# Kernel optimization log

Hardware: AMD Instinct MI355X
Metric: run time of the kernel (lower is better)

Reference implementation:

```python
import jax, jax.numpy as jnp
import numpy as np

B, S, D_IN = 2, 2048, 2048
H, KVH, HD = 32, 8, 64
GROUPS = H // KVH
EPS = 1e-6
SCALE = HD ** -0.5


def setup_inputs() -> dict:
    key = jax.random.key(0)
    ks = jax.random.split(key, 6)
    x = jax.random.normal(ks[0], (B, S, D_IN), jnp.float32)
    Wq = jax.random.normal(ks[1], (H * HD, D_IN), jnp.float32) * 0.02
    Wk = jax.random.normal(ks[2], (KVH * HD, D_IN), jnp.float32) * 0.02
    Wv = jax.random.normal(ks[3], (KVH * HD, D_IN), jnp.float32) * 0.02
    Wo = jax.random.normal(ks[4], (D_IN, H * HD), jnp.float32) * 0.02
    w_qnorm = jnp.ones((HD,), jnp.float32)
    w_knorm = jnp.ones((HD,), jnp.float32)
    # Llama-style RoPE tables: [S, HD] with frequencies duplicated across halves
    inv_freq = 1.0 / (10000.0 ** (np.arange(0, HD, 2, dtype=np.float32) / HD))
    ang = np.outer(np.arange(S, dtype=np.float32), inv_freq)  # [S, HD/2]
    emb = np.concatenate([ang, ang], axis=-1)  # [S, HD]
    cos = jnp.asarray(np.cos(emb), jnp.float32)
    sin = jnp.asarray(np.sin(emb), jnp.float32)
    mask = jnp.tril(jnp.ones((S, S), jnp.bool_))  # unused by module (causal hardcoded)
    return dict(x=x, mask=mask, cos=cos, sin=sin, Wq=Wq, Wk=Wk, Wv=Wv, Wo=Wo,
                w_qnorm=w_qnorm, w_knorm=w_knorm)


def _rms_norm(t, w):
    # per-head-dim RMSNorm, eps inside sqrt (torch nn.RMSNorm semantics)
    var = jnp.mean(jnp.square(t), axis=-1, keepdims=True)
    return t * jax.lax.rsqrt(var + EPS) * w


def _rotate_half(t):
    t1, t2 = jnp.split(t, 2, axis=-1)
    return jnp.concatenate([-t2, t1], axis=-1)


def _rope(t, cos, sin):
    # t: [B,H,S,HD]; cos/sin: [S,HD]
    return t * cos[None, None] + _rotate_half(t) * sin[None, None]


def reference(x, mask, cos, sin, Wq, Wk, Wv, Wo, w_qnorm, w_knorm):
    bs, seq, _ = x.shape
    q = (x @ Wq.T).reshape(bs, seq, H, HD).transpose(0, 2, 1, 3)    # [B,H,S,hd]
    k = (x @ Wk.T).reshape(bs, seq, KVH, HD).transpose(0, 2, 1, 3)  # [B,KVH,S,hd]
    v = (x @ Wv.T).reshape(bs, seq, KVH, HD).transpose(0, 2, 1, 3)
    # GQA: repeat_interleave KV over head dim
    k = jnp.repeat(k, GROUPS, axis=1)
    v = jnp.repeat(v, GROUPS, axis=1)
    # fused QK RMSNorm then RoPE
    q = _rope(_rms_norm(q, w_qnorm), cos, sin)
    k = _rope(_rms_norm(k, w_knorm), cos, sin)
    # causal attention
    scores = jnp.einsum('bhqd,bhkd->bhqk', q, k) * SCALE
    causal = jnp.arange(seq)[:, None] >= jnp.arange(seq)[None, :]
    scores = jnp.where(causal, scores, jnp.finfo(scores.dtype).min)
    attn = jax.nn.softmax(scores, axis=-1)
    out = jnp.einsum('bhqk,bhkd->bhqd', attn, v)
    out = out.transpose(0, 2, 1, 3).reshape(bs, seq, H * HD)
    return out @ Wo.T
```

## Files before the change

### kernel.cpp

```cpp
#include <hip/hip_runtime.h>

typedef __bf16 bf16_t;
typedef __bf16 bf16x8 __attribute__((ext_vector_type(8)));
typedef __bf16 bf16x4 __attribute__((ext_vector_type(4)));
typedef float f32x4 __attribute__((ext_vector_type(4)));
typedef unsigned int u32;

#define AS1 __attribute__((address_space(1)))
#define AS3 __attribute__((address_space(3)))

#define ASTR 72

#if __has_builtin(__builtin_amdgcn_exp2f)
#define EXP2(x) __builtin_amdgcn_exp2f(x)
#else
#define EXP2(x) exp2f(x)
#endif

__device__ __forceinline__ void g2l16(const bf16_t* g, bf16_t* l) {
  __builtin_amdgcn_global_load_lds((const AS1 u32*)g, (AS3 u32*)l, 16, 0, 0);
}

__device__ __forceinline__ u32 pkbf(float a, float b) {
  u32 ua = __builtin_bit_cast(u32, a) + 0x8000u;
  u32 ub = __builtin_bit_cast(u32, b) + 0x8000u;
  return (ua >> 16) | (ub & 0xFFFF0000u);
}

__global__ __launch_bounds__(256) void cvt5(
    const float* __restrict__ s0, const float* __restrict__ s1,
    const float* __restrict__ s2, const float* __restrict__ s3,
    const float* __restrict__ s4,
    bf16_t* __restrict__ d0, bf16_t* __restrict__ d1, bf16_t* __restrict__ d2,
    bf16_t* __restrict__ d3, bf16_t* __restrict__ d4)
{
  int blk = blockIdx.x;
  const float* s; bf16_t* d; int off;
  if      (blk <  8192) { s = s0; d = d0; off = blk;         }
  else if (blk < 12288) { s = s1; d = d1; off = blk -  8192; }
  else if (blk < 13312) { s = s2; d = d2; off = blk - 12288; }
  else if (blk < 14336) { s = s3; d = d3; off = blk - 13312; }
  else                  { s = s4; d = d4; off = blk - 14336; }
  size_t i = (size_t)off * 1024 + threadIdx.x * 4;
  float4 v = *(const float4*)&s[i];
  bf16x4 t;
  t[0] = (bf16_t)v.x; t[1] = (bf16_t)v.y; t[2] = (bf16_t)v.z; t[3] = (bf16_t)v.w;
  *(bf16x4*)&d[i] = t;
}

__device__ __forceinline__ void gemm_core(
    const bf16_t* __restrict__ A, const bf16_t* __restrict__ B, int K,
    bf16_t* As0, bf16_t* As1, bf16_t* Bs0, bf16_t* Bs1, f32x4 (&acc)[4][4])
{
  const int tid = threadIdx.x, lane = tid & 63, w = tid >> 6;
  const int col = lane & 15, quad = lane >> 4;
  const int wm = w >> 1, wn = w & 1;
  const int lr = lane >> 2;
  const int lc = (((lane & 3) ^ ((lane >> 3) & 3)) << 3);
  const int sw = ((quad ^ ((col >> 1) & 3)) << 3);
  const bf16_t* ga = A + (size_t)(w * 16 + lr) * K + lc;
  const bf16_t* gb = B + (size_t)(w * 16 + lr) * K + lc;
  const int lo0 = (w * 16) * 32, lo1 = (64 + w * 16) * 32;

  g2l16(ga,                  As0 + lo0);
  g2l16(ga + (size_t)64 * K, As0 + lo1);
  g2l16(gb,                  Bs0 + lo0);
  g2l16(gb + (size_t)64 * K, Bs0 + lo1);

  const int nkb = K >> 5;
  for (int kb = 0; kb < nkb; ++kb) {
    __syncthreads();
    bf16_t* Ac = (kb & 1) ? As1 : As0;
    bf16_t* Bc = (kb & 1) ? Bs1 : Bs0;
    if (kb + 1 < nkb) {
      bf16_t* An = (kb & 1) ? As0 : As1;
      bf16_t* Bn = (kb & 1) ? Bs0 : Bs1;
      const int k2 = (kb + 1) * 32;
      g2l16(ga + k2,                  An + lo0);
      g2l16(ga + k2 + (size_t)64 * K, An + lo1);
      g2l16(gb + k2,                  Bn + lo0);
      g2l16(gb + k2 + (size_t)64 * K, Bn + lo1);
    }

    bf16x8 af[4], bfr[4];
#pragma unroll
    for (int mt = 0; mt < 4; ++mt)
      af[mt] = *(const bf16x8*)&Ac[(wm * 64 + mt * 16 + col) * 32 + sw];
#pragma unroll
    for (int nt = 0; nt < 4; ++nt)
      bfr[nt] = *(const bf16x8*)&Bc[(wn * 64 + nt * 16 + col) * 32 + sw];
#pragma unroll
    for (int mt = 0; mt < 4; ++mt)
#pragma unroll
      for (int nt = 0; nt < 4; ++nt)
        acc[mt][nt] = __builtin_amdgcn_mfma_f32_16x16x32_bf16(af[mt], bfr[nt], acc[mt][nt], 0, 0, 0);
  }
}

__global__ __launch_bounds__(256, 4) void gemm_qkv(
    const bf16_t* __restrict__ xb, const bf16_t* __restrict__ Wqb,
    const bf16_t* __restrict__ Wkb, const bf16_t* __restrict__ Wvb,
    const float* __restrict__ cosT, const float* __restrict__ sinT,
    const float* __restrict__ wq, const float* __restrict__ wk,
    bf16_t* __restrict__ Qn, bf16_t* __restrict__ Kn, bf16_t* __restrict__ Vp)
{
  __shared__ bf16_t As[2][128 * 32], Bs[2][128 * 32];
  const int bn = blockIdx.x, bm = blockIdx.y;
  const bf16_t* B;
  if      (bn < 16) B = Wqb + (size_t)bn * 128 * 2048;
  else if (bn < 20) B = Wkb + (size_t)(bn - 16) * 128 * 2048;
  else              B = Wvb + (size_t)(bn - 20) * 128 * 2048;

  f32x4 acc[4][4] = {};
  gemm_core(xb + (size_t)bm * 128 * 2048, B, 2048, As[0], As[1], Bs[0], Bs[1], acc);

  const int lane = threadIdx.x & 63, w = threadIdx.x >> 6;
  const int col = lane & 15, quad = lane >> 4, wm = w >> 1, wn = w & 1;

  if (bn < 20) {
    const bool isQ = bn < 16;
    const float* wnv = isQ ? wq : wk;
    float w4[4];
#pragma unroll
    for (int nt = 0; nt < 4; ++nt) w4[nt] = wnv[nt * 16 + col];
    bf16_t* dst = isQ ? Qn + ((size_t)(bn * 2 + wn)) * 2048 * 64
                      : Kn + ((size_t)((bn - 16) * 2 + wn)) * 2048 * 64;
    const size_t bstride = isQ ? (size_t)32 * 2048 * 64 : (size_t)8 * 2048 * 64;
    const float qscale = 0.125f * 1.4426950408889634f;

#pragma unroll
    for (int mt = 0; mt < 4; ++mt)
#pragma unroll
      for (int r = 0; r < 4; ++r) {
        int row = bm * 128 + wm * 64 + mt * 16 + quad * 4 + r;
        int b = row >> 11, s = row & 2047;
        float v[4], ss = 0.f;
#pragma unroll
        for (int nt = 0; nt < 4; ++nt) { v[nt] = acc[mt][nt][r]; ss += v[nt] * v[nt]; }
        ss += __shfl_xor(ss, 1, 64);
        ss += __shfl_xor(ss, 2, 64);
        ss += __shfl_xor(ss, 4, 64);
        ss += __shfl_xor(ss, 8, 64);
        float rr = rsqrtf(ss * (1.0f / 64.0f) + 1e-6f);
        float t[4];
#pragma unroll
        for (int nt = 0; nt < 4; ++nt) t[nt] = v[nt] * rr * w4[nt];
        bf16_t* drow = dst + b * bstride + (size_t)s * 64;
#pragma unroll
        for (int nt = 0; nt < 4; ++nt) {
          int hd = nt * 16 + col;
          float rot = (nt < 2) ? -t[nt + 2] : t[nt - 2];
          float ov = t[nt] * cosT[s * 64 + hd] + rot * sinT[s * 64 + hd];
          if (isQ) ov *= qscale;
          drow[hd] = (bf16_t)ov;
        }
      }
  } else {
    const int cb = (bn - 20) * 128;
#pragma unroll
    for (int mt = 0; mt < 4; ++mt)
#pragma unroll
      for (int r = 0; r < 4; ++r) {
        int row = bm * 128 + wm * 64 + mt * 16 + quad * 4 + r;
        bf16_t* crow = Vp + (size_t)row * 512 + cb + wn * 64 + col;
#pragma unroll
        for (int nt = 0; nt < 4; ++nt)
          crow[nt * 16] = (bf16_t)acc[mt][nt][r];
      }
  }
}

__global__ __launch_bounds__(256, 4) void gemm_o(
    const bf16_t* __restrict__ Ao, const bf16_t* __restrict__ Wob,
    float* __restrict__ Cf)
{
  __shared__ bf16_t As[2][128 * 32], Bs[2][128 * 32];
  const int bn = blockIdx.x, bm = blockIdx.y;
  f32x4 acc[4][4] = {};
  gemm_core(Ao + (size_t)bm * 128 * 2048, Wob + (size_t)bn * 128 * 2048, 2048,
            As[0], As[1], Bs[0], Bs[1], acc);

  const int lane = threadIdx.x & 63, w = threadIdx.x >> 6;
  const int col = lane & 15, quad = lane >> 4, wm = w >> 1, wn = w & 1;
#pragma unroll
  for (int mt = 0; mt < 4; ++mt)
#pragma unroll
    for (int r = 0; r < 4; ++r) {
      int row = bm * 128 + wm * 64 + mt * 16 + quad * 4 + r;
      float* crow = Cf + (size_t)row * 2048 + bn * 128 + wn * 64 + col;
#pragma unroll
      for (int nt = 0; nt < 4; ++nt)
        crow[nt * 16] = acc[mt][nt][r];
    }
}

__global__ __launch_bounds__(256) void vtrans(
    const bf16_t* __restrict__ Vp, bf16_t* __restrict__ Vt)
{
  __shared__ bf16_t T[64 * 136];
  const int st = blockIdx.x, kvh = blockIdx.y, b = blockIdx.z;
  const int tid = threadIdx.x;
#pragma unroll
  for (int p = 0; p < 4; ++p) {
    int r = p * 32 + (tid >> 3);
    int c = (tid & 7) * 8;
    bf16x8 v = *(const bf16x8*)&Vp[((size_t)(b * 2048 + st * 128 + r)) * 512 + kvh * 64 + c];
#pragma unroll
    for (int i = 0; i < 8; ++i) T[(c + i) * 136 + r] = v[i];
  }
  __syncthreads();
#pragma unroll
  for (int p = 0; p < 4; ++p) {
    int hd = p * 16 + (tid >> 4);
    int sc = (tid & 15) * 8;
    bf16x8 v = *(const bf16x8*)&T[hd * 136 + sc];
    *(bf16x8*)&Vt[((size_t)((b * 8 + kvh) * 64) + hd) * 2048 + st * 128 + sc] = v;
  }
}

__global__ __launch_bounds__(256, 3) void attn(
    const bf16_t* __restrict__ Qn, const bf16_t* __restrict__ Kn,
    const bf16_t* __restrict__ Vt, bf16_t* __restrict__ Ao)
{
  __shared__ bf16_t KsL[2][64 * 32], KsH[2][64 * 32];
  __shared__ bf16_t VsL[2][64 * 32], VsH[2][64 * 32];
  __shared__ bf16_t Ps[128 * ASTR];

  const int tid = threadIdx.x, lane = tid & 63, w = tid >> 6;
  const int col = lane & 15, quad = lane >> 4;
  const int lr = lane >> 2;
  const int lcs = (((lane & 3) ^ ((lane >> 3) & 3)) << 3);
  const int sw  = ((quad ^ ((col >> 1) & 3)) << 3);
  const int h = blockIdx.x, b = blockIdx.y;
  const int qt = 15 - blockIdx.z;
  const int kvh = h >> 2;

  const bf16_t* Kb = Kn + ((size_t)(b * 8 + kvh)) * 2048 * 64;
  const bf16_t* Vb = Vt + ((size_t)(b * 8 + kvh)) * 64 * 2048;
  const bf16_t* Qb = Qn + (((size_t)(b * 32 + h)) * 2048 + qt * 128) * 64;
  const int lw = w * 512;

  bf16x8 Qf[2][2];
#pragma unroll
  for (int mt = 0; mt < 2; ++mt)
#pragma unroll
    for (int kk = 0; kk < 2; ++kk)
      Qf[mt][kk] = *(const bf16x8*)&Qb[(w * 32 + mt * 16 + col) * 64 + kk * 32 + quad * 8];

  bf16x8 ones;
#pragma unroll
  for (int i = 0; i < 8; ++i) ones[i] = (bf16_t)1.0f;

  f32x4 o[2][4] = {};
  f32x4 lacc[2] = {};

  const int rowmin = qt * 128 + w * 32;
  const int rowmax = rowmin + 31;
  const int jmax = 2 * qt + 1;

  {
    const bf16_t* gk = &Kb[(size_t)(w * 16 + lr) * 64 + lcs];
    const bf16_t* gv = &Vb[(size_t)(w * 16 + lr) * 2048 + lcs];
    g2l16(gk,      &KsL[0][lw]);
    g2l16(gk + 32, &KsH[0][lw]);
    g2l16(gv,      &VsL[0][lw]);
    g2l16(gv + 32, &VsH[0][lw]);
  }

  for (int j = 0; j <= jmax; ++j) {
    __syncthreads();
    if (j < jmax) {
      const int nb = (j + 1) & 1;
      const bf16_t* gk = &Kb[(size_t)((j + 1) * 64 + w * 16 + lr) * 64 + lcs];
      const bf16_t* gv = &Vb[(size_t)(w * 16 + lr) * 2048 + (j + 1) * 64 + lcs];
      g2l16(gk,      &KsL[nb][lw]);
      g2l16(gk + 32, &KsH[nb][lw]);
      g2l16(gv,      &VsL[nb][lw]);
      g2l16(gv + 32, &VsH[nb][lw]);
    }

    if (j * 64 <= rowmax) {
      const int bf = j & 1;
      const bool needmask = (j * 64 + 63 > rowmin);

#pragma unroll
      for (int kt = 0; kt < 4; ++kt) {
        bf16x8 kf0 = *(const bf16x8*)&KsL[bf][(kt * 16 + col) * 32 + sw];
        bf16x8 kf1 = *(const bf16x8*)&KsH[bf][(kt * 16 + col) * 32 + sw];
        f32x4 st0 = {}, st1 = {};
        st0 = __builtin_amdgcn_mfma_f32_16x16x32_bf16(kf0, Qf[0][0], st0, 0, 0, 0);
        st0 = __builtin_amdgcn_mfma_f32_16x16x32_bf16(kf1, Qf[0][1], st0, 0, 0, 0);
        st1 = __builtin_amdgcn_mfma_f32_16x16x32_bf16(kf0, Qf[1][0], st1, 0, 0, 0);
        st1 = __builtin_amdgcn_mfma_f32_16x16x32_bf16(kf1, Qf[1][1], st1, 0, 0, 0);
        const int k0 = j * 64 + kt * 16 + quad * 4;
#pragma unroll
        for (int mt = 0; mt < 2; ++mt) {
          f32x4 st = mt ? st1 : st0;
          float p0 = EXP2(st[0]), p1 = EXP2(st[1]);
          float p2 = EXP2(st[2]), p3 = EXP2(st[3]);
          if (needmask) {
            const int qg = qt * 128 + w * 32 + mt * 16 + col;
            p0 = (k0 + 0 > qg) ? 0.f : p0;
            p1 = (k0 + 1 > qg) ? 0.f : p1;
            p2 = (k0 + 2 > qg) ? 0.f : p2;
            p3 = (k0 + 3 > qg) ? 0.f : p3;
          }
          uint2 pk = { pkbf(p0, p1), pkbf(p2, p3) };
          *(uint2*)&Ps[(w * 32 + mt * 16 + col) * ASTR + kt * 16 + quad * 4] = pk;
        }
      }
      asm volatile("s_waitcnt lgkmcnt(0)" ::: "memory");

#pragma unroll
      for (int kk = 0; kk < 2; ++kk) {
        const bf16_t* Vh = kk ? &VsH[bf][0] : &VsL[bf][0];
        bf16x8 pa0 = *(const bf16x8*)&Ps[(w * 32 + col) * ASTR + kk * 32 + quad * 8];
        bf16x8 pa1 = *(const bf16x8*)&Ps[(w * 32 + 16 + col) * ASTR + kk * 32 + quad * 8];
        lacc[0] = __builtin_amdgcn_mfma_f32_16x16x32_bf16(pa0, ones, lacc[0], 0, 0, 0);
        lacc[1] = __builtin_amdgcn_mfma_f32_16x16x32_bf16(pa1, ones, lacc[1], 0, 0, 0);
#pragma unroll
        for (int nt = 0; nt < 4; ++nt) {
          bf16x8 vf = *(const bf16x8*)&Vh[(nt * 16 + col) * 32 + sw];
          o[0][nt] = __builtin_amdgcn_mfma_f32_16x16x32_bf16(pa0, vf, o[0][nt], 0, 0, 0);
          o[1][nt] = __builtin_amdgcn_mfma_f32_16x16x32_bf16(pa1, vf, o[1][nt], 0, 0, 0);
        }
      }
    }
  }

#pragma unroll
  for (int mt = 0; mt < 2; ++mt)
#pragma unroll
    for (int r = 0; r < 4; ++r) {
      float inv = 1.0f / lacc[mt][r];
      int row = b * 2048 + qt * 128 + w * 32 + mt * 16 + quad * 4 + r;
      bf16_t* orow = &Ao[(size_t)row * 2048 + h * 64 + col];
#pragma unroll
      for (int nt = 0; nt < 4; ++nt)
        orow[nt * 16] = (bf16_t)(o[mt][nt][r] * inv);
    }
}

extern "C" void kernel_launch(void* const* d_in, const int* in_sizes, int n_in,
                              void* d_out, int out_size, void* d_ws, size_t ws_size,
                              hipStream_t stream)
{
  const float* x    = (const float*)d_in[0];
  const float* cosT = (const float*)d_in[2];
  const float* sinT = (const float*)d_in[3];
  const float* Wq   = (const float*)d_in[4];
  const float* Wk   = (const float*)d_in[5];
  const float* Wv   = (const float*)d_in[6];
  const float* Wo   = (const float*)d_in[7];
  const float* wq   = (const float*)d_in[8];
  const float* wk   = (const float*)d_in[9];
  float* out = (float*)d_out;

  char* ws = (char*)d_ws;
  bf16_t* xb  = (bf16_t*)(ws);
  bf16_t* Ao  = (bf16_t*)(ws);
  bf16_t* Wqb = (bf16_t*)(ws + 16777216);
  bf16_t* Vt  = (bf16_t*)(ws + 16777216);
  bf16_t* Wkb = (bf16_t*)(ws + 25165824);
  bf16_t* Wvb = (bf16_t*)(ws + 27262976);
  bf16_t* Wob = (bf16_t*)(ws + 29360128);
  bf16_t* Vp  = (bf16_t*)(ws + 37748736);
  bf16_t* Qn  = (bf16_t*)(ws + 41943040);
  bf16_t* Kn  = (bf16_t*)(ws + 58720256);

  cvt5<<<18432, 256, 0, stream>>>(x, Wq, Wk, Wv, Wo, xb, Wqb, Wkb, Wvb, Wob);
  gemm_qkv<<<dim3(24, 32), 256, 0, stream>>>(xb, Wqb, Wkb, Wvb, cosT, sinT, wq, wk, Qn, Kn, Vp);
  vtrans<<<dim3(16, 8, 2), 256, 0, stream>>>(Vp, Vt);
  attn<<<dim3(32, 2, 16), 256, 0, stream>>>(Qn, Kn, Vt, Ao);
  gemm_o<<<dim3(16, 32), 256, 0, stream>>>(Ao, Wob, out);
}
```

Baseline: 296.7 us.

## Fuse V transpose into QKV GEMM epilogue and process two heads per attention block

The QKV GEMM epilogue now writes V directly in the transposed [b,kvh,hd,s] layout using 4-element bf16 stores, which removes the separate vtrans kernel and its extra global round trip. The attention kernel now handles two query heads that share a KV head in each block. Each K/V tile loaded into LDS is reused for both heads, halving the grid and the K/V traffic per head. In exchange the kernel needs more registers (launch bounds lowered to 2 blocks per CU), the grid is smaller, and the V stores are narrower and strided.

```diff
diff --git a/kernel.cpp b/kernel.cpp
--- a/kernel.cpp
+++ b/kernel.cpp
@@ -102,7 +102,7 @@
     const bf16_t* __restrict__ Wkb, const bf16_t* __restrict__ Wvb,
     const float* __restrict__ cosT, const float* __restrict__ sinT,
     const float* __restrict__ wq, const float* __restrict__ wk,
-    bf16_t* __restrict__ Qn, bf16_t* __restrict__ Kn, bf16_t* __restrict__ Vp)
+    bf16_t* __restrict__ Qn, bf16_t* __restrict__ Kn, bf16_t* __restrict__ Vt)
 {
   __shared__ bf16_t As[2][128 * 32], Bs[2][128 * 32];
   const int bn = blockIdx.x, bm = blockIdx.y;
@@ -156,17 +156,19 @@
         }
       }
   } else {
-    const int cb = (bn - 20) * 128;
-#pragma unroll
-    for (int mt = 0; mt < 4; ++mt)
-#pragma unroll
-      for (int r = 0; r < 4; ++r) {
-        int row = bm * 128 + wm * 64 + mt * 16 + quad * 4 + r;
-        bf16_t* crow = Vp + (size_t)row * 512 + cb + wn * 64 + col;
-#pragma unroll
-        for (int nt = 0; nt < 4; ++nt)
-          crow[nt * 16] = (bf16_t)acc[mt][nt][r];
-      }
+    const int kvh = (bn - 20) * 2 + wn;
+#pragma unroll
+    for (int mt = 0; mt < 4; ++mt) {
+      int row0 = bm * 128 + wm * 64 + mt * 16 + quad * 4;
+      int b = row0 >> 11, s0 = row0 & 2047;
+#pragma unroll
+      for (int nt = 0; nt < 4; ++nt) {
+        bf16x4 t;
+#pragma unroll
+        for (int r = 0; r < 4; ++r) t[r] = (bf16_t)acc[mt][nt][r];
+        *(bf16x4*)&Vt[(((size_t)(b * 8 + kvh)) * 64 + nt * 16 + col) * 2048 + s0] = t;
+      }
+    }
   }
 }
 
@@ -194,31 +196,7 @@
     }
 }
 
-__global__ __launch_bounds__(256) void vtrans(
-    const bf16_t* __restrict__ Vp, bf16_t* __restrict__ Vt)
-{
-  __shared__ bf16_t T[64 * 136];
-  const int st = blockIdx.x, kvh = blockIdx.y, b = blockIdx.z;
-  const int tid = threadIdx.x;
-#pragma unroll
-  for (int p = 0; p < 4; ++p) {
-    int r = p * 32 + (tid >> 3);
-    int c = (tid & 7) * 8;
-    bf16x8 v = *(const bf16x8*)&Vp[((size_t)(b * 2048 + st * 128 + r)) * 512 + kvh * 64 + c];
-#pragma unroll
-    for (int i = 0; i < 8; ++i) T[(c + i) * 136 + r] = v[i];
-  }
-  __syncthreads();
-#pragma unroll
-  for (int p = 0; p < 4; ++p) {
-    int hd = p * 16 + (tid >> 4);
-    int sc = (tid & 15) * 8;
-    bf16x8 v = *(const bf16x8*)&T[hd * 136 + sc];
-    *(bf16x8*)&Vt[((size_t)((b * 8 + kvh) * 64) + hd) * 2048 + st * 128 + sc] = v;
-  }
-}
-
-__global__ __launch_bounds__(256, 3) void attn(
+__global__ __launch_bounds__(256, 2) void attn(
     const bf16_t* __restrict__ Qn, const bf16_t* __restrict__ Kn,
     const bf16_t* __restrict__ Vt, bf16_t* __restrict__ Ao)
 {
@@ -231,28 +209,32 @@
   const int lr = lane >> 2;
   const int lcs = (((lane & 3) ^ ((lane >> 3) & 3)) << 3);
   const int sw  = ((quad ^ ((col >> 1) & 3)) << 3);
-  const int h = blockIdx.x, b = blockIdx.y;
+  const int hp = blockIdx.x, b = blockIdx.y;
   const int qt = 15 - blockIdx.z;
-  const int kvh = h >> 2;
+  const int h0 = hp * 2;
+  const int kvh = h0 >> 2;
 
   const bf16_t* Kb = Kn + ((size_t)(b * 8 + kvh)) * 2048 * 64;
   const bf16_t* Vb = Vt + ((size_t)(b * 8 + kvh)) * 64 * 2048;
-  const bf16_t* Qb = Qn + (((size_t)(b * 32 + h)) * 2048 + qt * 128) * 64;
+  const bf16_t* Qb = Qn + (((size_t)(b * 32 + h0)) * 2048 + qt * 128) * 64;
   const int lw = w * 512;
 
-  bf16x8 Qf[2][2];
-#pragma unroll
-  for (int mt = 0; mt < 2; ++mt)
-#pragma unroll
-    for (int kk = 0; kk < 2; ++kk)
-      Qf[mt][kk] = *(const bf16x8*)&Qb[(w * 32 + mt * 16 + col) * 64 + kk * 32 + quad * 8];
+  bf16x8 Qf[2][2][2];
+#pragma unroll
+  for (int hh = 0; hh < 2; ++hh)
+#pragma unroll
+    for (int mt = 0; mt < 2; ++mt)
+#pragma unroll
+      for (int kk = 0; kk < 2; ++kk)
+        Qf[hh][mt][kk] = *(const bf16x8*)&Qb[(size_t)hh * 2048 * 64 +
+                                             (w * 32 + mt * 16 + col) * 64 + kk * 32 + quad * 8];
 
   bf16x8 ones;
 #pragma unroll
   for (int i = 0; i < 8; ++i) ones[i] = (bf16_t)1.0f;
 
-  f32x4 o[2][4] = {};
-  f32x4 lacc[2] = {};
+  f32x4 o[2][2][4] = {};
+  f32x4 lacc[2][2] = {};
 
   const int rowmin = qt * 128 + w * 32;
   const int rowmax = rowmin + 31;
@@ -283,62 +265,84 @@
       const int bf = j & 1;
       const bool needmask = (j * 64 + 63 > rowmin);
 
+      u32 pk[2][2][4][2];
 #pragma unroll
       for (int kt = 0; kt < 4; ++kt) {
         bf16x8 kf0 = *(const bf16x8*)&KsL[bf][(kt * 16 + col) * 32 + sw];
         bf16x8 kf1 = *(const bf16x8*)&KsH[bf][(kt * 16 + col) * 32 + sw];
-        f32x4 st0 = {}, st1 = {};
-        st0 = __builtin_amdgcn_mfma_f32_16x16x32_bf16(kf0, Qf[0][0], st0, 0, 0, 0);
-        st0 = __builtin_amdgcn_mfma_f32_16x16x32_bf16(kf1, Qf[0][1], st0, 0, 0, 0);
-        st1 = __builtin_amdgcn_mfma_f32_16x16x32_bf16(kf0, Qf[1][0], st1, 0, 0, 0);
-        st1 = __builtin_amdgcn_mfma_f32_16x16x32_bf16(kf1, Qf[1][1], st1, 0, 0, 0);
         const int k0 = j * 64 + kt * 16 + quad * 4;
 #pragma unroll
-        for (int mt = 0; mt < 2; ++mt) {
-          f32x4 st = mt ? st1 : st0;
-          float p0 = EXP2(st[0]), p1 = EXP2(st[1]);
-          float p2 = EXP2(st[2]), p3 = EXP2(st[3]);
-          if (needmask) {
-            const int qg = qt * 128 + w * 32 + mt * 16 + col;
-            p0 = (k0 + 0 > qg) ? 0.f : p0;
-            p1 = (k0 + 1 > qg) ? 0.f : p1;
-            p2 = (k0 + 2 > qg) ? 0.f : p2;
-            p3 = (k0 + 3 > qg) ? 0.f : p3;
+        for (int hh = 0; hh < 2; ++hh)
+#pragma unroll
+          for (int mt = 0; mt < 2; ++mt) {
+            f32x4 st = {};
+            st = __builtin_amdgcn_mfma_f32_16x16x32_bf16(kf0, Qf[hh][mt][0], st, 0, 0, 0);
+            st = __builtin_amdgcn_mfma_f32_16x16x32_bf16(kf1, Qf[hh][mt][1], st, 0, 0, 0);
+            float p0 = EXP2(st[0]), p1 = EXP2(st[1]);
+            float p2 = EXP2(st[2]), p3 = EXP2(st[3]);
+            if (needmask) {
+              const int qg = qt * 128 + w * 32 + mt * 16 + col;
+              p0 = (k0 + 0 > qg) ? 0.f : p0;
+              p1 = (k0 + 1 > qg) ? 0.f : p1;
+              p2 = (k0 + 2 > qg) ? 0.f : p2;
+              p3 = (k0 + 3 > qg) ? 0.f : p3;
+            }
+            pk[hh][mt][kt][0] = pkbf(p0, p1);
+            pk[hh][mt][kt][1] = pkbf(p2, p3);
           }
-          uint2 pk = { pkbf(p0, p1), pkbf(p2, p3) };
-          *(uint2*)&Ps[(w * 32 + mt * 16 + col) * ASTR + kt * 16 + quad * 4] = pk;
-        }
-      }
-      asm volatile("s_waitcnt lgkmcnt(0)" ::: "memory");
-
+      }
+
+      bf16x8 vf[2][4];
 #pragma unroll
       for (int kk = 0; kk < 2; ++kk) {
         const bf16_t* Vh = kk ? &VsH[bf][0] : &VsL[bf][0];
-        bf16x8 pa0 = *(const bf16x8*)&Ps[(w * 32 + col) * ASTR + kk * 32 + quad * 8];
-        bf16x8 pa1 = *(const bf16x8*)&Ps[(w * 32 + 16 + col) * ASTR + kk * 32 + quad * 8];
-        lacc[0] = __builtin_amdgcn_mfma_f32_16x16x32_bf16(pa0, ones, lacc[0], 0, 0, 0);
-        lacc[1] = __builtin_amdgcn_mfma_f32_16x16x32_bf16(pa1, ones, lacc[1], 0, 0, 0);
-#pragma unroll
-        for (int nt = 0; nt < 4; ++nt) {
-          bf16x8 vf = *(const bf16x8*)&Vh[(nt * 16 + col) * 32 + sw];
-          o[0][nt] = __builtin_amdgcn_mfma_f32_16x16x32_bf16(pa0, vf, o[0][nt], 0, 0, 0);
-          o[1][nt] = __builtin_amdgcn_mfma_f32_16x16x32_bf16(pa1, vf, o[1][nt], 0, 0, 0);
+#pragma unroll
+        for (int nt = 0; nt < 4; ++nt)
+          vf[kk][nt] = *(const bf16x8*)&Vh[(nt * 16 + col) * 32 + sw];
+      }
+
+#pragma unroll
+      for (int hh = 0; hh < 2; ++hh) {
+#pragma unroll
+        for (int mt = 0; mt < 2; ++mt)
+#pragma unroll
+          for (int kt = 0; kt < 4; ++kt) {
+            uint2 u = { pk[hh][mt][kt][0], pk[hh][mt][kt][1] };
+            *(uint2*)&Ps[(w * 32 + mt * 16 + col) * ASTR + kt * 16 + quad * 4] = u;
+          }
+        asm volatile("s_waitcnt lgkmcnt(0)" ::: "memory");
+
+#pragma unroll
+        for (int kk = 0; kk < 2; ++kk) {
+          bf16x8 pa0 = *(const bf16x8*)&Ps[(w * 32 + col) * ASTR + kk * 32 + quad * 8];
+          bf16x8 pa1 = *(const bf16x8*)&Ps[(w * 32 + 16 + col) * ASTR + kk * 32 + quad * 8];
+          lacc[hh][0] = __builtin_amdgcn_mfma_f32_16x16x32_bf16(pa0, ones, lacc[hh][0], 0, 0, 0);
+          lacc[hh][1] = __builtin_amdgcn_mfma_f32_16x16x32_bf16(pa1, ones, lacc[hh][1], 0, 0, 0);
+#pragma unroll
+          for (int nt = 0; nt < 4; ++nt) {
+            o[hh][0][nt] = __builtin_amdgcn_mfma_f32_16x16x32_bf16(pa0, vf[kk][nt], o[hh][0][nt], 0, 0, 0);
+            o[hh][1][nt] = __builtin_amdgcn_mfma_f32_16x16x32_bf16(pa1, vf[kk][nt], o[hh][1][nt], 0, 0, 0);
+          }
         }
+        if (hh == 0)
+          asm volatile("s_waitcnt lgkmcnt(0)" ::: "memory");
       }
     }
   }
 
 #pragma unroll
-  for (int mt = 0; mt < 2; ++mt)
-#pragma unroll
-    for (int r = 0; r < 4; ++r) {
-      float inv = 1.0f / lacc[mt][r];
-      int row = b * 2048 + qt * 128 + w * 32 + mt * 16 + quad * 4 + r;
-      bf16_t* orow = &Ao[(size_t)row * 2048 + h * 64 + col];
-#pragma unroll
-      for (int nt = 0; nt < 4; ++nt)
-        orow[nt * 16] = (bf16_t)(o[mt][nt][r] * inv);
-    }
+  for (int hh = 0; hh < 2; ++hh)
+#pragma unroll
+    for (int mt = 0; mt < 2; ++mt)
+#pragma unroll
+      for (int r = 0; r < 4; ++r) {
+        float inv = 1.0f / lacc[hh][mt][r];
+        int row = b * 2048 + qt * 128 + w * 32 + mt * 16 + quad * 4 + r;
+        bf16_t* orow = &Ao[(size_t)row * 2048 + (h0 + hh) * 64 + col];
+#pragma unroll
+        for (int nt = 0; nt < 4; ++nt)
+          orow[nt * 16] = (bf16_t)(o[hh][mt][nt][r] * inv);
+      }
 }
 
 extern "C" void kernel_launch(void* const* d_in, const int* in_sizes, int n_in,
@@ -360,17 +364,15 @@
   bf16_t* xb  = (bf16_t*)(ws);
   bf16_t* Ao  = (bf16_t*)(ws);
   bf16_t* Wqb = (bf16_t*)(ws + 16777216);
-  bf16_t* Vt  = (bf16_t*)(ws + 16777216);
   bf16_t* Wkb = (bf16_t*)(ws + 25165824);
   bf16_t* Wvb = (bf16_t*)(ws + 27262976);
   bf16_t* Wob = (bf16_t*)(ws + 29360128);
-  bf16_t* Vp  = (bf16_t*)(ws + 37748736);
+  bf16_t* Vt  = (bf16_t*)(ws + 37748736);
   bf16_t* Qn  = (bf16_t*)(ws + 41943040);
   bf16_t* Kn  = (bf16_t*)(ws + 58720256);
 
   cvt5<<<18432, 256, 0, stream>>>(x, Wq, Wk, Wv, Wo, xb, Wqb, Wkb, Wvb, Wob);
-  gemm_qkv<<<dim3(24, 32), 256, 0, stream>>>(xb, Wqb, Wkb, Wvb, cosT, sinT, wq, wk, Qn, Kn, Vp);
-  vtrans<<<dim3(16, 8, 2), 256, 0, stream>>>(Vp, Vt);
-  attn<<<dim3(32, 2, 16), 256, 0, stream>>>(Qn, Kn, Vt, Ao);
+  gemm_qkv<<<dim3(24, 32), 256, 0, stream>>>(xb, Wqb, Wkb, Wvb, cosT, sinT, wq, wk, Qn, Kn, Vt);
+  attn<<<dim3(16, 2, 16), 256, 0, stream>>>(Qn, Kn, Vt, Ao);
   gemm_o<<<dim3(16, 32), 256, 0, stream>>>(Ao, Wob, out);
 }
```

Result: slower. 325.4 us (+9.7%).
